# Kernel tuning notes

Measured on AMD Instinct MI355X. Metric: run time of the kernel, lower is better.

## Reference

```python
import jax, jax.numpy as jnp
import numpy as np
import math

B, C1, H, W, D, NH = 32, 128, 32, 32, 256, 8
KS = 9
GLOBAL_RATIO = 0.0005
K_CH = 8


def setup_inputs() -> dict:
    key = jax.random.key(0)
    ks = jax.random.split(key, 6)
    s = 1.0 / math.sqrt(D)
    return {
        "x": jax.random.normal(ks[0], (B, 1, H, W), jnp.float32),
        "conv_w": jax.random.normal(ks[1], (C1, 1, KS, KS), jnp.float32) * 0.05,
        "channel_embed": jax.random.normal(ks[2], (C1, D), jnp.float32),
        "in_proj_w": jax.random.normal(ks[3], (3 * D, D), jnp.float32) * s,
        "in_proj_b": jnp.zeros((3 * D,), jnp.float32),
        "out_proj_w": jax.random.normal(ks[4], (D, D), jnp.float32) * s,
        "out_proj_b": jnp.zeros((D,), jnp.float32),
    }


def _pos_encoding(h, w, d):
    # Faithful to the torch code: the (H, d/2) sin/cos source broadcasts against
    # the trailing (W, d/2) dims of the (H,W,d/2) slice, so the PE varies only
    # along the W axis (requires H == W, which holds here).
    div = jnp.exp(jnp.arange(0, d, 2, dtype=jnp.float32) * (-math.log(10000.0) / d))
    ang = jnp.arange(w, dtype=jnp.float32)[:, None] * div          # (W, d/2)
    pe_w = jnp.stack([jnp.sin(ang), jnp.cos(ang)], axis=-1).reshape(w, d)
    return jnp.broadcast_to(pe_w[None], (h, w, d))                 # (H, W, d)


def _forward(x, conv_w, channel_embed, in_proj_w, in_proj_b, out_proj_w, out_proj_b):
    A = jax.nn.relu(jax.lax.conv_general_dilated(
        x, conv_w, window_strides=(1, 1),
        padding=[(KS // 2, KS // 2), (KS // 2, KS // 2)],
        dimension_numbers=("NCHW", "OIHW", "NCHW")))                # (B,C,H,W)
    Bb, C, Hh, Ww = A.shape
    k = max(1, int(math.ceil(GLOBAL_RATIO * C * Hh * Ww)))          # = 66

    # global top-k threshold mask over flattened activations
    A_flat = A.reshape(Bb, -1)
    topk_vals, _ = jax.lax.top_k(A_flat, k)
    thresh = topk_vals[:, -1][:, None]
    mask_global = (A_flat >= thresh).reshape(A.shape)
    A_global = A * mask_global.astype(A.dtype)

    # per-pixel channel top-8 + scatter
    v = jnp.transpose(A_global, (0, 2, 3, 1))                       # (B,H,W,C)
    topv, topi = jax.lax.top_k(v, K_CH)                             # (B,H,W,8)
    logits = (jax.nn.one_hot(topi, C, dtype=v.dtype) * topv[..., None]).sum(axis=-2)

    # global max normalization per batch element
    gmax = jnp.max(logits.reshape(Bb, -1), axis=1)[:, None, None, None]
    denom = jnp.where(gmax == 0, jnp.float32(1.0), gmax)
    sparse_weights = jnp.where(gmax == 0, jnp.float32(0.0), logits / denom)

    # channel-embedding projection + 2D positional encoding
    loc_emb = jnp.einsum('bhwc,cd->bhwd', sparse_weights, channel_embed)
    loc_emb = loc_emb + _pos_encoding(Hh, Ww, D)[None]
    seq = loc_emb.reshape(Bb, Hh * Ww, D)                           # (B, S, D)

    # nn.MultiheadAttention (batch_first) self-attention
    qkv = seq @ in_proj_w.T + in_proj_b
    q, kk, vv = jnp.split(qkv, 3, axis=-1)
    dh = D // NH
    heads = lambda t: t.reshape(Bb, -1, NH, dh).transpose(0, 2, 1, 3)
    q, kk, vv = heads(q), heads(kk), heads(vv)
    scores = jnp.einsum('bhqd,bhkd->bhqk', q, kk) / math.sqrt(dh)
    attn = jax.nn.softmax(scores, axis=-1)
    ctx = jnp.einsum('bhqk,bhkd->bhqd', attn, vv)
    ctx = ctx.transpose(0, 2, 1, 3).reshape(Bb, -1, D)
    attn_out = ctx @ out_proj_w.T + out_proj_b                      # (B, S, D)

    pooled = attn_out.mean(axis=1)                                  # (B, D)
    return pooled, sparse_weights, topi


def reference(x, conv_w, channel_embed, in_proj_w, in_proj_b, out_proj_w, out_proj_b):
    return _forward(x, conv_w, channel_embed, in_proj_w, in_proj_b,
                    out_proj_w, out_proj_b)
```

## Files before the change

kernel.cpp:

```cpp
#include <hip/hip_runtime.h>
#include <hip/hip_bf16.h>

#define BB 32
#define C1 128
#define SS 1024
#define DD 256
#define NHH 8
#define DHH 32
#define KSEL 66
#define TRIPLE 768
#define NTOK 80
#define SCAPS 128
#define CCAP 2048
#define DMAX (32 + NTOK)
#define PEROW (BB * NTOK)
#define SELFLAG 0x40000000u

typedef __attribute__((ext_vector_type(8))) short bf16x8;
typedef __attribute__((ext_vector_type(4))) float f32x4;

__device__ inline short f2bf(float f) {
  union { __hip_bfloat16 h; unsigned short u; } c;
  c.h = __float2bfloat16(f);
  return (short)c.u;
}
__device__ inline float pe_val(int w, int d) {
  int i2 = d >> 1;
  float dv = expf((float)(2 * i2) * (-9.210340371976184f / 256.f));
  float ang = (float)w * dv;
  return (d & 1) ? cosf(ang) : sinf(ang);
}

__global__ __launch_bounds__(256) void conv_relu_hist_kernel(
    const float* __restrict__ x, const float* __restrict__ w, float* __restrict__ A,
    unsigned* __restrict__ ghist1, unsigned* __restrict__ gmaxb,
    float* __restrict__ out_topi) {
  const int bx = blockIdx.x;
  const int b = bx >> 6, c0 = (bx & 63) * 2;
  __shared__ float xs[40 * 40];
  __shared__ unsigned h[2048];
  __shared__ unsigned smax;
  const int t = threadIdx.x;
  if (bx < 256) {
    int k0 = bx * 1024 + t * 4;
    float4 v = (k0 & 4) ? make_float4(4.f, 5.f, 6.f, 7.f)
                        : make_float4(0.f, 1.f, 2.f, 3.f);
    *(float4*)&out_topi[k0] = v;
  }
  for (int i = t; i < 1600; i += 256) {
    int r = i / 40, cc = i - r * 40;
    int gi = r - 4, gj = cc - 4;
    float v = 0.f;
    if (gi >= 0 && gi < 32 && gj >= 0 && gj < 32) v = x[(size_t)b * 1024 + gi * 32 + gj];
    xs[i] = v;
  }
  for (int i = t; i < 2048; i += 256) h[i] = 0u;
  if (t == 0) smax = 0u;
  __syncthreads();
  const float* w0 = w + (size_t)c0 * 81;
  const float* w1 = w0 + 81;
  const int r = t >> 3, cbase = (t & 7) * 4;
  const float4* xs4 = (const float4*)xs;
  float a0 = 0.f, a1 = 0.f, a2 = 0.f, a3 = 0.f;
  float b0 = 0.f, b1 = 0.f, b2 = 0.f, b3 = 0.f;
#pragma unroll
  for (int u = 0; u < 9; ++u) {
    int base4 = (r + u) * 10 + (t & 7);
    float4 xA = xs4[base4];
    float4 xB = xs4[base4 + 1];
    float4 xC = xs4[base4 + 2];
    float xv[12] = {xA.x, xA.y, xA.z, xA.w, xB.x, xB.y, xB.z, xB.w,
                    xC.x, xC.y, xC.z, xC.w};
#pragma unroll
    for (int v = 0; v < 9; ++v) {
      float f0 = w0[u * 9 + v], f1 = w1[u * 9 + v];
      a0 += f0 * xv[v];     a1 += f0 * xv[v + 1];
      a2 += f0 * xv[v + 2]; a3 += f0 * xv[v + 3];
      b0 += f1 * xv[v];     b1 += f1 * xv[v + 1];
      b2 += f1 * xv[v + 2]; b3 += f1 * xv[v + 3];
    }
  }
  a0 = fmaxf(a0, 0.f); a1 = fmaxf(a1, 0.f); a2 = fmaxf(a2, 0.f); a3 = fmaxf(a3, 0.f);
  b0 = fmaxf(b0, 0.f); b1 = fmaxf(b1, 0.f); b2 = fmaxf(b2, 0.f); b3 = fmaxf(b3, 0.f);
  float4 va = {a0, a1, a2, a3}, vb = {b0, b1, b2, b3};
  *(float4*)&A[((size_t)(b * C1 + c0) << 10) + r * 32 + cbase] = va;
  *(float4*)&A[((size_t)(b * C1 + c0 + 1) << 10) + r * 32 + cbase] = vb;
  unsigned lmax = 0u;
#pragma unroll
  for (int k = 0; k < 8; ++k) {
    float f = (k == 0) ? a0 : (k == 1) ? a1 : (k == 2) ? a2 : (k == 3) ? a3
            : (k == 4) ? b0 : (k == 5) ? b1 : (k == 6) ? b2 : b3;
    unsigned bits = __float_as_uint(f);
    if (bits > lmax) lmax = bits;
    if (bits >= (1u << 21)) atomicAdd(&h[bits >> 21], 1u);
  }
  atomicMax(&smax, lmax);
  __syncthreads();
  for (int i = t; i < 2048; i += 256)
    if (h[i]) atomicAdd(&ghist1[b * 2048 + i], h[i]);
  if (t == 0) atomicMax(&gmaxb[b], smax);
}

__global__ __launch_bounds__(1024) void sel_kernel(
    const unsigned* __restrict__ gh, unsigned* __restrict__ selv,
    unsigned* __restrict__ cnd_n, float* __restrict__ ctx) {
  const int b = blockIdx.x, t = threadIdx.x;
  __shared__ unsigned hl[2048];
  __shared__ unsigned sfx[1024];
  if (t < 256) ctx[b * DD + t] = 0.f;
  if (t == 0) cnd_n[b * 32] = 0u;
  unsigned r = (unsigned)KSEL;
  hl[t] = gh[b * 2048 + t];
  hl[t + 1024] = gh[b * 2048 + t + 1024];
  __syncthreads();
  sfx[t] = hl[2 * t] + hl[2 * t + 1];
  __syncthreads();
  for (int off = 1; off < 1024; off <<= 1) {
    unsigned v = (t + off < 1024) ? sfx[t + off] : 0u;
    __syncthreads();
    sfx[t] += v;
    __syncthreads();
  }
  if (sfx[0] < r) {
    if (t == 0) selv[b] = SELFLAG;
    return;
  }
  unsigned Snext = (t < 1023) ? sfx[t + 1] : 0u;
  unsigned hi = hl[2 * t + 1], lo = hl[2 * t];
  if (Snext < r && Snext + hi >= r) selv[b] = (unsigned)(2 * t + 1);
  else if (Snext + hi < r && Snext + hi + lo >= r) selv[b] = (unsigned)(2 * t);
}

__global__ __launch_bounds__(256) void gather_kernel(
    const float* __restrict__ A, const unsigned* __restrict__ selv,
    unsigned* __restrict__ cnd_n, float* __restrict__ candv,
    unsigned* __restrict__ candloc) {
  const int b = blockIdx.y, slice = blockIdx.x, t = threadIdx.x;
  const unsigned v1 = selv[b];
  if (v1 == SELFLAG) return;
  const unsigned thr = v1 << 21;
  __shared__ float lv[512];
  __shared__ unsigned ll[512];
  __shared__ unsigned lcnt, gbase;
  if (t == 0) lcnt = 0u;
  __syncthreads();
  const float4* Ab = (const float4*)(A + (size_t)b * (C1 * SS) + slice * 2048);
  const float4 va = Ab[t];
  const float4 vb = Ab[t + 256];
  const int base = slice * 2048 + t * 4;
  const float f[8] = {va.x, va.y, va.z, va.w, vb.x, vb.y, vb.z, vb.w};
#pragma unroll
  for (int c = 0; c < 8; ++c) {
    if (__float_as_uint(f[c]) >= thr) {
      unsigned loc = (unsigned)(base + (c < 4 ? c : 1020 + c));
      unsigned s = atomicAdd(&lcnt, 1u);
      if (s < 512u) {
        lv[s] = f[c];
        ll[s] = loc;
      } else {
        unsigned g = atomicAdd(&cnd_n[b * 32], 1u);
        if (g < (unsigned)CCAP) {
          candv[b * CCAP + g] = f[c];
          candloc[b * CCAP + g] = loc;
        }
      }
    }
  }
  __syncthreads();
  const unsigned cnt = lcnt < 512u ? lcnt : 512u;
  if (t == 0 && cnt) gbase = atomicAdd(&cnd_n[b * 32], cnt);
  __syncthreads();
  for (unsigned u = t; u < cnt; u += 256) {
    unsigned s = gbase + u;
    if (s < (unsigned)CCAP) {
      candv[b * CCAP + s] = lv[u];
      candloc[b * CCAP + s] = ll[u];
    }
  }
}

__global__ __launch_bounds__(256) void sparse_pixels_kernel(
    const unsigned* __restrict__ cnd_n, const float* __restrict__ candv,
    const unsigned* __restrict__ candloc, const unsigned* __restrict__ selv,
    const float* __restrict__ gmaxp, float* __restrict__ out_sw,
    float* __restrict__ out_topi, int* __restrict__ kidx8,
    float* __restrict__ kval8, unsigned* __restrict__ glist,
    unsigned* __restrict__ nswb, unsigned* __restrict__ npix) {
  const int b = blockIdx.x, t = threadIdx.x;
  __shared__ float cv[CCAP];
  __shared__ unsigned cl[CCAP];
  __shared__ float sv[SCAPS];
  __shared__ int sch[SCAPS], spx[SCAPS];
  __shared__ int s_n_sh;
  __shared__ unsigned pixbit[32];
  __shared__ int mcount[NTOK];
  __shared__ int leadp[NTOK];
  if (t == 0) s_n_sh = 0;
  if (t < 32) pixbit[t] = 0u;
  unsigned n = cnd_n[b * 32];
  if (n > (unsigned)CCAP) n = (unsigned)CCAP;
  const bool ok = (selv[b] != SELFLAG) && (n >= (unsigned)KSEL);
  for (unsigned i = t; i < n; i += 256) {
    cv[i] = candv[b * CCAP + i];
    cl[i] = candloc[b * CCAP + i];
  }
  __syncthreads();
  if (ok) {
    for (unsigned i = t; i < n; i += 256) {
      float v = cv[i];
      int g = 0;
      for (unsigned j = 0; j < n; ++j) g += (cv[j] > v);
      if (g < KSEL) {
        int k = atomicAdd(&s_n_sh, 1);
        if (k < SCAPS) {
          sv[k] = v;
          sch[k] = (int)(cl[i] >> 10);
          spx[k] = (int)(cl[i] & 1023u);
        }
      }
    }
  }
  __syncthreads();
  const int s_n = s_n_sh < SCAPS ? s_n_sh : SCAPS;
  for (int i = t; i < s_n; i += 256)
    atomicOr(&pixbit[spx[i] >> 5], 1u << (spx[i] & 31));
  __syncthreads();
  if (t == 0) {
    int np = 0;
#pragma unroll
    for (int wd = 0; wd < 32; ++wd) np += __popc(pixbit[wd]);
    npix[b] = (unsigned)(np < NTOK ? np : NTOK);
  }
  if (t < 32) {
    unsigned cnt = 0;
#pragma unroll
    for (int rr = 0; rr < 32; ++rr) cnt += (pixbit[rr] >> t) & 1u;
    nswb[b * 32 + t] = cnt;
  }
  const float gm = gmaxp[b];
  const float scale = gm > 0.f ? 1.f / gm : 0.f;
  __syncthreads();
  for (int i = t; i < s_n; i += 256) {
    const int p = spx[i];
    const float v = sv[i];
    const int c = sch[i];
    const int word = p >> 5, bit = p & 31;
    int slot = 0;
    for (int wd = 0; wd < word; ++wd) slot += __popc(pixbit[wd]);
    slot += __popc(pixbit[word] & (bit ? ((1u << bit) - 1u) : 0u));
    if (slot >= NTOK) continue;
    int rank = 0, cntp = 0;
    for (int j = 0; j < s_n; ++j) {
      if (spx[j] != p) continue;
      ++cntp;
      rank += (sv[j] > v || (sv[j] == v && sch[j] < c));
    }
    const size_t pix = (size_t)b * SS + p;
    const float sval = v * scale;
    if (rank < 8) {
      out_topi[pix * 8 + rank] = (float)c;
      out_sw[pix * C1 + c] = sval;
      kidx8[((size_t)b * NTOK + slot) * 8 + rank] = c;
      kval8[((size_t)b * NTOK + slot) * 8 + rank] = sval;
    }
    if (rank == 0) {
      glist[b * NTOK + slot] =
          ((unsigned)b << 16) | ((unsigned)slot << 8) | (unsigned)(p & 31);
      mcount[slot] = cntp < 8 ? cntp : 8;
      leadp[slot] = p;
    }
  }
  __syncthreads();
  const int np = (int)npix[b];
  for (int s = t; s < np; s += 256) {
    const int m = mcount[s];
    if (m >= 8) continue;
    const int p = leadp[s];
    int used[8];
    for (int k = 0; k < m; ++k) used[k] = kidx8[((size_t)b * NTOK + s) * 8 + k];
    int fill_c = 0;
    for (int j = m; j < 8; ++j) {
      bool adv = true;
      while (adv) {
        adv = false;
        for (int k = 0; k < m; ++k)
          if (used[k] == fill_c) adv = true;
        if (adv) ++fill_c;
      }
      kidx8[((size_t)b * NTOK + s) * 8 + j] = fill_c;
      kval8[((size_t)b * NTOK + s) * 8 + j] = 0.f;
      out_topi[((size_t)b * SS + p) * 8 + j] = (float)fill_c;
      ++fill_c;
    }
  }
}

__global__ __launch_bounds__(256) void emb_build_kernel(
    const unsigned* __restrict__ npix, const int* __restrict__ kidx8,
    const float* __restrict__ kval8, const unsigned* __restrict__ glist,
    const float* __restrict__ emb, float* __restrict__ E) {
  const int bx = blockIdx.x;
  const int d = threadIdx.x;
  if (bx >= PEROW) {
    E[(size_t)bx * DD + d] = pe_val(bx - PEROW, d);
    return;
  }
  const int b = bx / NTOK, i = bx - b * NTOK;
  if ((unsigned)i >= npix[b]) return;
  const int w = (int)(glist[bx] & 255u);
  const int* ki = kidx8 + (size_t)bx * 8;
  const float* kv = kval8 + (size_t)bx * 8;
  float e = pe_val(w, d);
#pragma unroll
  for (int j = 0; j < 8; ++j) e += kv[j] * emb[(size_t)ki[j] * DD + d];
  E[(size_t)bx * DD + d] = e;
}

__global__ __launch_bounds__(256) void eqkv_gemm_kernel(
    const float* __restrict__ E, const float* __restrict__ W,
    const float* __restrict__ bias, float* __restrict__ SQKV) {
  __shared__ __align__(16) short As[128][40];
  __shared__ __align__(16) short Bs[128][40];
  const int mt = blockIdx.x / 6, nt = blockIdx.x % 6;
  const int t = threadIdx.x;
  const int wv = t >> 6, lane = t & 63, lg = lane >> 4, ln = lane & 15;
  const int wm = wv >> 1, wn = wv & 1;

  f32x4 acc[4][4];
#pragma unroll
  for (int i = 0; i < 4; ++i)
#pragma unroll
    for (int j = 0; j < 4; ++j) acc[i][j] = (f32x4){0, 0, 0, 0};

  for (int k0 = 0; k0 < DD; k0 += 32) {
    __syncthreads();
    for (int f = t; f < 1024; f += 256) {
      int row = f >> 3, q4 = (f & 7) * 4;
      float4 xa = *(const float4*)&E[(size_t)(mt * 128 + row) * DD + k0 + q4];
      float4 wa = *(const float4*)&W[(size_t)(nt * 128 + row) * DD + k0 + q4];
      short* ad = &As[row][q4];
      ad[0] = f2bf(xa.x); ad[1] = f2bf(xa.y); ad[2] = f2bf(xa.z); ad[3] = f2bf(xa.w);
      short* bd = &Bs[row][q4];
      bd[0] = f2bf(wa.x); bd[1] = f2bf(wa.y); bd[2] = f2bf(wa.z); bd[3] = f2bf(wa.w);
    }
    __syncthreads();
    bf16x8 af[4], bfr[4];
#pragma unroll
    for (int i = 0; i < 4; ++i) af[i] = *(const bf16x8*)&As[wm * 64 + i * 16 + ln][lg * 8];
#pragma unroll
    for (int j = 0; j < 4; ++j) bfr[j] = *(const bf16x8*)&Bs[wn * 64 + j * 16 + ln][lg * 8];
#pragma unroll
    for (int i = 0; i < 4; ++i)
#pragma unroll
      for (int j = 0; j < 4; ++j)
        acc[i][j] = __builtin_amdgcn_mfma_f32_16x16x32_bf16(af[i], bfr[j], acc[i][j], 0, 0, 0);
  }
#pragma unroll
  for (int i = 0; i < 4; ++i) {
#pragma unroll
    for (int j = 0; j < 4; ++j) {
      int col = nt * 128 + wn * 64 + j * 16 + ln;
      float bcol = bias[col];
#pragma unroll
      for (int r = 0; r < 4; ++r) {
        int row = mt * 128 + wm * 64 + i * 16 + lg * 4 + r;
        SQKV[(size_t)row * TRIPLE + col] = acc[i][j][r] + bcol;
      }
    }
  }
}

__global__ __launch_bounds__(256) void attn_small_kernel(
    const float* __restrict__ SQKV, const unsigned* __restrict__ npix,
    const unsigned* __restrict__ nswb, float* __restrict__ ctx_sum) {
  const int blk = blockIdx.x;
  const int qg = blk & 3, h = (blk >> 2) & 7, b = blk >> 5;
  const int nsb = (int)npix[b];
  const int D = 32 + nsb;
  if (qg * 32 >= D) return;
  const int t = threadIdx.x;
  __shared__ float Kh[DMAX][36];
  __shared__ float Vh[DMAX][36];
  __shared__ float cw[DMAX];
  __shared__ float sctx[32];
  const int hoff = h * DHH;
  for (int idx = t; idx < D * 32; idx += 256) {
    int j = idx >> 5, d = idx & 31;
    int row = (j < 32) ? (PEROW + j) : (b * NTOK + j - 32);
    const float* src = &SQKV[(size_t)row * TRIPLE];
    Kh[j][d] = src[DD + hoff + d];
    Vh[j][d] = src[2 * DD + hoff + d];
  }
  if (t < D) cw[t] = (t < 32) ? (float)(32 - (int)nswb[b * 32 + t]) : 1.0f;
  if (t < 32) sctx[t] = 0.f;
  __syncthreads();

  const int q = qg * 32 + (t >> 3);
  const int g = t & 7;
  const bool act = (q < D);
  float m = -1e30f, l = 0.f;
  float acc[32];
#pragma unroll
  for (int d = 0; d < 32; ++d) acc[d] = 0.f;
  if (act) {
    const float qsc = 0.25506973f;
    int qrow = (q < 32) ? (PEROW + q) : (b * NTOK + q - 32);
    const float* qsrc = &SQKV[(size_t)qrow * TRIPLE];
    float qv[32];
#pragma unroll
    for (int d = 0; d < 32; ++d) qv[d] = qsrc[hoff + d] * qsc;
#pragma unroll 1
    for (int j = g; j < D; j += 8) {
      float s = 0.f;
      const float* kr = &Kh[j][0];
#pragma unroll
      for (int d = 0; d < 32; ++d) s += qv[d] * kr[d];
      float mn = fmaxf(m, s);
      float corr = exp2f(m - mn);
      float pw = cw[j] * exp2f(s - mn);
      l = l * corr + pw;
      const float* vr = &Vh[j][0];
#pragma unroll
      for (int d = 0; d < 32; ++d) acc[d] = acc[d] * corr + pw * vr[d];
      m = mn;
    }
  }
#pragma unroll
  for (int off = 1; off <= 4; off <<= 1) {
    float mo = __shfl_xor(m, off);
    float lo = __shfl_xor(l, off);
    float mm = fmaxf(m, mo);
    float fa = exp2f(m - mm), fb = exp2f(mo - mm);
    l = l * fa + lo * fb;
#pragma unroll
    for (int d = 0; d < 32; ++d) {
      float ao = __shfl_xor(acc[d], off);
      acc[d] = acc[d] * fa + ao * fb;
    }
    m = mm;
  }
  const float wq = (act && l > 0.f) ? cw[q] / l : 0.f;
#pragma unroll
  for (int d = 0; d < 32; ++d) {
    float val = wq * acc[d];
    val += __shfl_xor(val, 8);
    val += __shfl_xor(val, 16);
    val += __shfl_xor(val, 32);
    if ((t & 63) == 0) atomicAdd(&sctx[d], val);
  }
  __syncthreads();
  if (t < 32) atomicAdd(&ctx_sum[b * DD + hoff + t], sctx[t]);
}

__global__ __launch_bounds__(256) void pooled_kernel(
    const float* __restrict__ ctx_sum, const float* __restrict__ Wout,
    const float* __restrict__ bout, float* __restrict__ out) {
  const int b = blockIdx.x;
  const int o = threadIdx.x;
  __shared__ float mc[DD];
  mc[o] = ctx_sum[b * DD + o] * (1.f / 1024.f);
  __syncthreads();
  float acc = bout[o];
  const float* wr = Wout + (size_t)o * DD;
#pragma unroll 4
  for (int d = 0; d < DD; ++d) acc += mc[d] * wr[d];
  out[b * DD + o] = acc;
}

extern "C" void kernel_launch(void* const* d_in, const int* in_sizes, int n_in,
                              void* d_out, int out_size, void* d_ws, size_t ws_size,
                              hipStream_t stream) {
  const float* x = (const float*)d_in[0];
  const float* conv_w = (const float*)d_in[1];
  const float* emb = (const float*)d_in[2];
  const float* ipw = (const float*)d_in[3];
  const float* ipb = (const float*)d_in[4];
  const float* opw = (const float*)d_in[5];
  const float* opb = (const float*)d_in[6];

  float* out = (float*)d_out;
  float* out_pooled = out;
  float* out_sw = out + 8192;
  float* out_topi = out + 8192 + 4194304;

  char* ws = (char*)d_ws;
  float*    A      = (float*)(ws);
  unsigned* ghist1 = (unsigned*)(ws + 16777216);
  unsigned* selv   = (unsigned*)(ws + 17039360);
  unsigned* gmaxb  = (unsigned*)(ws + 17039488);
  unsigned* nswb   = (unsigned*)(ws + 17039616);
  unsigned* npix   = (unsigned*)(ws + 17043712);
  unsigned* glist  = (unsigned*)(ws + 17043840);
  unsigned* cnd_n  = (unsigned*)(ws + 17054080);
  float*    candv  = (float*)(ws + 17058176);
  unsigned* candloc= (unsigned*)(ws + 17320320);
  int*      kidx8  = (int*)(ws + 17582464);
  float*    kval8  = (float*)(ws + 17664384);
  float*    E      = (float*)(ws + 17746304);
  float*    SQKV   = (float*)(ws + 20498816);
  float*    ctx    = (float*)(ws + 28756352);

  hipMemsetAsync(out_sw, 0, (size_t)4194304 * 4, stream);
  hipMemsetAsync(ws + 16777216, 0, 262400, stream);

  conv_relu_hist_kernel<<<BB * 64, 256, 0, stream>>>(x, conv_w, A, ghist1, gmaxb, out_topi);
  sel_kernel<<<BB, 1024, 0, stream>>>(ghist1, selv, cnd_n, ctx);
  gather_kernel<<<dim3(64, BB), 256, 0, stream>>>(A, selv, cnd_n, candv, candloc);
  sparse_pixels_kernel<<<BB, 256, 0, stream>>>(cnd_n, candv, candloc, selv,
                                               (const float*)gmaxb, out_sw, out_topi,
                                               kidx8, kval8, glist, nswb, npix);
  emb_build_kernel<<<PEROW + 32, 256, 0, stream>>>(npix, kidx8, kval8, glist, emb, E);
  eqkv_gemm_kernel<<<21 * 6, 256, 0, stream>>>(E, ipw, ipb, SQKV);
  attn_small_kernel<<<BB * NHH * 4, 256, 0, stream>>>(SQKV, npix, nswb, ctx);
  pooled_kernel<<<BB, 256, 0, stream>>>(ctx, opw, opb, out_pooled);
}
```

Measured before the change: 132.3 us.

## Fold memsets into conv kernel and replace global histogram atomics with private histograms

Removes the two hipMemsetAsync calls. The conv kernel now zeroes the sparse-weights output itself and computes the positional-encoding rows of E that emb_build_kernel used to produce. Each conv block writes its full 2048-bin histogram and max to a private slot instead of doing global atomics. sel_kernel then reduces the 64 per-block histograms per batch, which adds about 16 MB of extra writes and reads in exchange for no atomics and no memsets.

```diff
diff --git a/kernel.cpp b/kernel.cpp
--- a/kernel.cpp
+++ b/kernel.cpp
@@ -33,20 +33,28 @@
 
 __global__ __launch_bounds__(256) void conv_relu_hist_kernel(
     const float* __restrict__ x, const float* __restrict__ w, float* __restrict__ A,
-    unsigned* __restrict__ ghist1, unsigned* __restrict__ gmaxb,
-    float* __restrict__ out_topi) {
+    unsigned* __restrict__ ghist_priv, unsigned* __restrict__ gmaxpriv,
+    float* __restrict__ out_topi, float* __restrict__ out_sw,
+    float* __restrict__ E) {
   const int bx = blockIdx.x;
   const int b = bx >> 6, c0 = (bx & 63) * 2;
   __shared__ float xs[40 * 40];
   __shared__ unsigned h[2048];
   __shared__ unsigned smax;
   const int t = threadIdx.x;
+  {
+    float4 z = {0.f, 0.f, 0.f, 0.f};
+    float4* sw4 = (float4*)(out_sw + (size_t)bx * 2048);
+    sw4[t] = z;
+    sw4[t + 256] = z;
+  }
   if (bx < 256) {
     int k0 = bx * 1024 + t * 4;
     float4 v = (k0 & 4) ? make_float4(4.f, 5.f, 6.f, 7.f)
                         : make_float4(0.f, 1.f, 2.f, 3.f);
     *(float4*)&out_topi[k0] = v;
   }
+  if (bx < 32) E[(size_t)(PEROW + bx) * DD + t] = pe_val(bx, t);
   for (int i = t; i < 1600; i += 256) {
     int r = i / 40, cc = i - r * 40;
     int gi = r - 4, gj = cc - 4;
@@ -96,23 +104,41 @@
   }
   atomicMax(&smax, lmax);
   __syncthreads();
-  for (int i = t; i < 2048; i += 256)
-    if (h[i]) atomicAdd(&ghist1[b * 2048 + i], h[i]);
-  if (t == 0) atomicMax(&gmaxb[b], smax);
+  {
+    uint4* dst = (uint4*)(ghist_priv + (size_t)bx * 2048);
+    const uint4* src = (const uint4*)h;
+    dst[t] = src[t];
+    dst[t + 256] = src[t + 256];
+  }
+  if (t == 0) gmaxpriv[bx] = smax;
 }
 
 __global__ __launch_bounds__(1024) void sel_kernel(
-    const unsigned* __restrict__ gh, unsigned* __restrict__ selv,
+    const unsigned* __restrict__ ghist_priv, const unsigned* __restrict__ gmaxpriv,
+    unsigned* __restrict__ selv, unsigned* __restrict__ gmaxb,
     unsigned* __restrict__ cnd_n, float* __restrict__ ctx) {
   const int b = blockIdx.x, t = threadIdx.x;
   __shared__ unsigned hl[2048];
   __shared__ unsigned sfx[1024];
+  __shared__ unsigned gmx;
   if (t < 256) ctx[b * DD + t] = 0.f;
-  if (t == 0) cnd_n[b * 32] = 0u;
+  if (t == 0) { cnd_n[b * 32] = 0u; gmx = 0u; }
+  __syncthreads();
+  if (t < 64) atomicMax(&gmx, gmaxpriv[b * 64 + t]);
+  {
+    const unsigned* base = ghist_priv + (size_t)b * 64 * 2048;
+    unsigned s0 = 0, s1 = 0;
+#pragma unroll 4
+    for (int s = 0; s < 64; ++s) {
+      s0 += base[s * 2048 + t];
+      s1 += base[s * 2048 + t + 1024];
+    }
+    hl[t] = s0;
+    hl[t + 1024] = s1;
+  }
+  __syncthreads();
+  if (t == 0) gmaxb[b] = gmx;
   unsigned r = (unsigned)KSEL;
-  hl[t] = gh[b * 2048 + t];
-  hl[t + 1024] = gh[b * 2048 + t + 1024];
-  __syncthreads();
   sfx[t] = hl[2 * t] + hl[2 * t + 1];
   __syncthreads();
   for (int off = 1; off < 1024; off <<= 1) {
@@ -301,10 +327,6 @@
     const float* __restrict__ emb, float* __restrict__ E) {
   const int bx = blockIdx.x;
   const int d = threadIdx.x;
-  if (bx >= PEROW) {
-    E[(size_t)bx * DD + d] = pe_val(bx - PEROW, d);
-    return;
-  }
   const int b = bx / NTOK, i = bx - b * NTOK;
   if ((unsigned)i >= npix[b]) return;
   const int w = (int)(glist[bx] & 255u);
@@ -484,32 +506,31 @@
   float* out_topi = out + 8192 + 4194304;
 
   char* ws = (char*)d_ws;
-  float*    A      = (float*)(ws);
-  unsigned* ghist1 = (unsigned*)(ws + 16777216);
-  unsigned* selv   = (unsigned*)(ws + 17039360);
-  unsigned* gmaxb  = (unsigned*)(ws + 17039488);
-  unsigned* nswb   = (unsigned*)(ws + 17039616);
-  unsigned* npix   = (unsigned*)(ws + 17043712);
-  unsigned* glist  = (unsigned*)(ws + 17043840);
-  unsigned* cnd_n  = (unsigned*)(ws + 17054080);
-  float*    candv  = (float*)(ws + 17058176);
-  unsigned* candloc= (unsigned*)(ws + 17320320);
-  int*      kidx8  = (int*)(ws + 17582464);
-  float*    kval8  = (float*)(ws + 17664384);
-  float*    E      = (float*)(ws + 17746304);
-  float*    SQKV   = (float*)(ws + 20498816);
-  float*    ctx    = (float*)(ws + 28756352);
-
-  hipMemsetAsync(out_sw, 0, (size_t)4194304 * 4, stream);
-  hipMemsetAsync(ws + 16777216, 0, 262400, stream);
-
-  conv_relu_hist_kernel<<<BB * 64, 256, 0, stream>>>(x, conv_w, A, ghist1, gmaxb, out_topi);
-  sel_kernel<<<BB, 1024, 0, stream>>>(ghist1, selv, cnd_n, ctx);
+  float*    A       = (float*)(ws);
+  unsigned* ghist_p = (unsigned*)(ws + 16777216);
+  unsigned* gmaxpriv= (unsigned*)(ws + 33554432);
+  unsigned* selv    = (unsigned*)(ws + 33562624);
+  unsigned* gmaxb   = (unsigned*)(ws + 33562752);
+  unsigned* nswb    = (unsigned*)(ws + 33562880);
+  unsigned* npix    = (unsigned*)(ws + 33566976);
+  unsigned* glist   = (unsigned*)(ws + 33567104);
+  unsigned* cnd_n   = (unsigned*)(ws + 33577344);
+  float*    candv   = (float*)(ws + 33581440);
+  unsigned* candloc = (unsigned*)(ws + 33843584);
+  int*      kidx8   = (int*)(ws + 34105728);
+  float*    kval8   = (float*)(ws + 34187648);
+  float*    E       = (float*)(ws + 34269568);
+  float*    SQKV    = (float*)(ws + 37022080);
+  float*    ctx     = (float*)(ws + 45279616);
+
+  conv_relu_hist_kernel<<<BB * 64, 256, 0, stream>>>(x, conv_w, A, ghist_p, gmaxpriv,
+                                                     out_topi, out_sw, E);
+  sel_kernel<<<BB, 1024, 0, stream>>>(ghist_p, gmaxpriv, selv, gmaxb, cnd_n, ctx);
   gather_kernel<<<dim3(64, BB), 256, 0, stream>>>(A, selv, cnd_n, candv, candloc);
   sparse_pixels_kernel<<<BB, 256, 0, stream>>>(cnd_n, candv, candloc, selv,
                                                (const float*)gmaxb, out_sw, out_topi,
                                                kidx8, kval8, glist, nswb, npix);
-  emb_build_kernel<<<PEROW + 32, 256, 0, stream>>>(npix, kidx8, kval8, glist, emb, E);
+  emb_build_kernel<<<PEROW, 256, 0, stream>>>(npix, kidx8, kval8, glist, emb, E);
   eqkv_gemm_kernel<<<21 * 6, 256, 0, stream>>>(E, ipw, ipb, SQKV);
   attn_small_kernel<<<BB * NHH * 4, 256, 0, stream>>>(SQKV, npix, nswb, ctx);
   pooled_kernel<<<BB, 256, 0, stream>>>(ctx, opw, opb, out_pooled);
```

New measurement: 120.4 us. -9.0%, faster.
